# Kernel optimization log

Hardware: AMD Instinct MI355X
Metric: run time of the kernel (lower is better)

Reference implementation:

```python
import jax, jax.numpy as jnp
import numpy as np

B = 8192
N_INPUT = 64
N_OUTPUT = 128
N_HIDDEN = 32
N_TARGETS = 2
N_EXOGS = 3
N_SERIES = N_TARGETS + N_EXOGS  # 5


def _init_linear(k, fan_in, w_shape, b_shape):
    # torch nn.Linear default init: U(-1/sqrt(fan_in), 1/sqrt(fan_in))
    bound = 1.0 / np.sqrt(fan_in)
    kw, kb = jax.random.split(k)
    W = jax.random.uniform(kw, w_shape, jnp.float32, -bound, bound)
    b = jax.random.uniform(kb, b_shape, jnp.float32, -bound, bound)
    return W, b


def setup_inputs() -> dict:
    key = jax.random.key(0)
    ks = jax.random.split(key, 5)
    target = jax.random.normal(ks[0], (B, N_INPUT, N_TARGETS), jnp.float32)
    exog = jax.random.normal(ks[1], (B, N_INPUT + N_OUTPUT, N_EXOGS), jnp.float32)
    # linear1: (n_input*n_series) -> n_targets
    W1, b1 = _init_linear(ks[2], N_INPUT * N_SERIES, (N_TARGETS, N_INPUT * N_SERIES), (N_TARGETS,))
    # linear2: n_series separate (n_input -> n_hidden) linears, stacked
    W2, b2 = _init_linear(ks[3], N_INPUT, (N_SERIES, N_HIDDEN, N_INPUT), (N_SERIES, N_HIDDEN))
    # linear3: (n_hidden*n_series) -> n_targets
    W3, b3 = _init_linear(ks[4], N_HIDDEN * N_SERIES, (N_TARGETS, N_HIDDEN * N_SERIES), (N_TARGETS,))
    return dict(target=target, exog=exog, W1=W1, b1=b1, W2=W2, b2=b2, W3=W3, b3=b3)


def _single_predict(window, ex, W1, b1, W2, b2, W3, b3):
    # window: (B, n_input, n_targets), ex: (B, n_input, n_exogs)
    te = jnp.concatenate([window, ex], axis=2)  # (B, n_input, n_series)
    flat = te.reshape(te.shape[0], -1)          # time-major, series fastest (torch Flatten order)
    out1 = flat @ W1.T + b1                     # (B, n_targets)
    # per-series tiny linears batched via einsum: h[b,i,:] = W2[i] @ te[b,:,i]
    h = jnp.einsum('bti,iht->bih', te, W2) + b2  # (B, n_series, n_hidden)
    h = jax.nn.sigmoid(h).reshape(h.shape[0], -1)  # series-major concat order matches torch.cat
    out2 = h @ W3.T + b3                        # (B, n_targets)
    return out1 + out2 + window[:, -1, :]


def reference(target, exog, W1, b1, W2, b2, W3, b3):
    def step(window, i):
        ex = jax.lax.dynamic_slice_in_dim(exog, i, N_INPUT, axis=1)  # (B, n_input, n_exogs)
        pred = _single_predict(window, ex, W1, b1, W2, b2, W3, b3)   # (B, n_targets)
        window = jnp.concatenate([window[:, 1:, :], pred[:, None, :]], axis=1)
        return window, pred

    _, preds = jax.lax.scan(step, target, jnp.arange(N_OUTPUT))
    return jnp.transpose(preds, (1, 0, 2))  # (B, n_output, n_targets)
```

## Files before the change

kernel.cpp:

```cpp
#include <hip/hip_runtime.h>
#include <math.h>

#define NB 8192
#define NIN 64
#define NOUT 128
#define NHID 32
#define NEXO 3
#define EXROWS 192
#define NTGT 2

typedef float f32x2 __attribute__((ext_vector_type(2)));
typedef float f32x4 __attribute__((ext_vector_type(4)));
typedef int   i32x4 __attribute__((ext_vector_type(4)));
typedef short bf16x8 __attribute__((ext_vector_type(8)));

__device__ __forceinline__ float sigmoidf(float x) {
    return 1.0f / (1.0f + __expf(-x));
}

__device__ __forceinline__ unsigned short f2bf(float x) {
    unsigned int u = __float_as_uint(x);
    unsigned int r = u + 0x7fffu + ((u >> 16) & 1u);
    return (unsigned short)(r >> 16);
}
__device__ __forceinline__ float bf2f(unsigned short h) {
    return __uint_as_float((unsigned int)h << 16);
}

template<int CTRL>
__device__ __forceinline__ float dpp_add(float x) {
    int p = __builtin_amdgcn_update_dpp(0, __float_as_int(x), CTRL, 0xf, 0xf, true);
    return x + __int_as_float(p);
}

#if __has_builtin(__builtin_amdgcn_permlane16_swap)
__device__ __forceinline__ f32x2 xchg16(f32x2 v, int s) {
    auto rx = __builtin_amdgcn_permlane16_swap(__float_as_uint(v.x), __float_as_uint(v.x), false, false);
    auto ry = __builtin_amdgcn_permlane16_swap(__float_as_uint(v.y), __float_as_uint(v.y), false, false);
    f32x2 r;
    r.x = s ? __uint_as_float(rx[0]) : __uint_as_float(rx[1]);
    r.y = s ? __uint_as_float(ry[0]) : __uint_as_float(ry[1]);
    return r;
}
#else
__device__ __forceinline__ f32x2 xchg16(f32x2 v, int s) {
    (void)s;
    f32x2 r;
    r.x = __int_as_float(__builtin_amdgcn_ds_swizzle(__float_as_int(v.x), 0x401f));
    r.y = __int_as_float(__builtin_amdgcn_ds_swizzle(__float_as_int(v.y), 0x401f));
    return r;
}
#endif

__device__ __forceinline__ f32x2 fold32(f32x2 v, int s32) {
    auto rx = __builtin_amdgcn_permlane32_swap(__float_as_uint(v.x), __float_as_uint(v.x), false, false);
    auto ry = __builtin_amdgcn_permlane32_swap(__float_as_uint(v.y), __float_as_uint(v.y), false, false);
    f32x2 o;
    o.x = v.x + (s32 ? __uint_as_float(rx[0]) : __uint_as_float(rx[1]));
    o.y = v.y + (s32 ? __uint_as_float(ry[0]) : __uint_as_float(ry[1]));
    return o;
}

__global__ __launch_bounds__(256, 4) void narx_exog_kernel(
    const float* __restrict__ exog,
    const float* __restrict__ W1, const float* __restrict__ b1,
    const float* __restrict__ W2, const float* __restrict__ b2,
    const float* __restrict__ W3, const float* __restrict__ b3,
    float* __restrict__ E)
{
    __shared__ __align__(16) float exs[NEXO][EXROWS];
    __shared__ __align__(16) unsigned short exrep[NEXO * 8][200];
    __shared__ __align__(16) unsigned short w2bf[NEXO * 32][72];
    __shared__ __align__(16) float2 w1e2[NEXO][NIN];
    __shared__ __align__(16) float b2l[96];
    __shared__ __align__(16) float w3l[2][96];

    const int tid = threadIdx.x;
    const int b = blockIdx.x;
    const float* exb = exog + (size_t)b * (EXROWS * NEXO);

    for (int idx = tid; idx < EXROWS * NEXO; idx += 256) {
        int t = idx / 3;
        int e = idx - t * 3;
        exs[e][t] = exb[idx];
    }
    for (int idx = tid; idx < 6144; idx += 256) {
        int e = idx >> 11;
        int rem = idx & 2047;
        int u = rem >> 6, t = rem & 63;
        w2bf[e * 32 + u][t] = f2bf(W2[(size_t)(64 + e * 32 + u) * NIN + t]);
    }
    for (int idx = tid; idx < 192; idx += 256) {
        int e = idx >> 6, t = idx & 63;
        w1e2[e][t] = make_float2(W1[t * 5 + 2 + e], W1[320 + t * 5 + 2 + e]);
    }
    if (tid < 96)  b2l[tid] = b2[64 + tid];
    for (int idx = tid; idx < 192; idx += 256) {
        int o = idx / 96, u = idx - o * 96;
        w3l[o][u] = W3[o * 160 + 64 + u];
    }
    __syncthreads();

    for (int idx = tid; idx < NEXO * 8 * 192; idx += 256) {
        int e = idx / 1536;
        int rem = idx - e * 1536;
        int r = rem / 192;
        int q = rem - r * 192;
        float v = (q + r < 192) ? exs[e][q + r] : 0.f;
        exrep[e * 8 + r][q] = f2bf(v);
    }
    __syncthreads();

    const int wv = tid >> 6;
    const int l  = tid & 63;
    const int iw = wv * 32;
    const int lg = l >> 4;
    const int col = l & 15;

    float acc0[2] = {0.f, 0.f};
    float acc1[2] = {0.f, 0.f};

    #pragma unroll 1
    for (int e = 0; e < NEXO; ++e) {
        f32x4 b2v[2], w30v[2], w31v[2];
        #pragma unroll
        for (int mt = 0; mt < 2; ++mt) {
            b2v[mt]  = *(const f32x4*)&b2l[e * 32 + mt * 16 + lg * 4];
            w30v[mt] = *(const f32x4*)&w3l[0][e * 32 + mt * 16 + lg * 4];
            w31v[mt] = *(const f32x4*)&w3l[1][e * 32 + mt * 16 + lg * 4];
        }

        f32x4 cacc[2][2];
        #pragma unroll
        for (int mt = 0; mt < 2; ++mt)
            #pragma unroll
            for (int nt = 0; nt < 2; ++nt)
                cacc[mt][nt] = b2v[mt];

        #pragma unroll
        for (int kt = 0; kt < 2; ++kt) {
            bf16x8 af[2], bfr[2];
            #pragma unroll
            for (int mt = 0; mt < 2; ++mt)
                af[mt] = *(const bf16x8*)&w2bf[e * 32 + mt * 16 + col][kt * 32 + lg * 8];
            #pragma unroll
            for (int nt = 0; nt < 2; ++nt)
                bfr[nt] = *(const bf16x8*)&exrep[e * 8 + (l & 7)]
                              [iw + nt * 16 + kt * 32 + lg * 8 + ((l >> 3) & 1) * 8];
            #pragma unroll
            for (int mt = 0; mt < 2; ++mt)
                #pragma unroll
                for (int nt = 0; nt < 2; ++nt)
                    cacc[mt][nt] = __builtin_amdgcn_mfma_f32_16x16x32_bf16(
                        af[mt], bfr[nt], cacc[mt][nt], 0, 0, 0);
        }

        #pragma unroll
        for (int mt = 0; mt < 2; ++mt)
            #pragma unroll
            for (int nt = 0; nt < 2; ++nt) {
                #pragma unroll
                for (int r = 0; r < 4; ++r) {
                    float sg = sigmoidf(cacc[mt][nt][r]);
                    acc0[nt] += w30v[mt][r] * sg;
                    acc1[nt] += w31v[mt][r] * sg;
                }
            }

        const float* exs_e = &exs[e][0];
        #pragma unroll
        for (int dt = 0; dt < 16; ++dt) {
            float2 wv2 = w1e2[e][lg * 16 + dt];
            float x0 = exs_e[iw + l + dt];
            float x1 = exs_e[iw + 16 + l + dt];
            acc0[0] += wv2.x * x0;
            acc1[0] += wv2.y * x0;
            acc0[1] += wv2.x * x1;
            acc1[1] += wv2.y * x1;
        }
    }

    #pragma unroll
    for (int nt = 0; nt < 2; ++nt) {
        acc0[nt] += __shfl_xor(acc0[nt], 16, 64);
        acc0[nt] += __shfl_xor(acc0[nt], 32, 64);
        acc1[nt] += __shfl_xor(acc1[nt], 16, 64);
        acc1[nt] += __shfl_xor(acc1[nt], 32, 64);
    }
    if (lg == 0) {
        const float bias0 = b1[0] + b3[0];
        const float bias1 = b1[1] + b3[1];
        #pragma unroll
        for (int nt = 0; nt < 2; ++nt) {
            int i = iw + nt * 16 + col;
            *(float2*)&E[(size_t)b * (NOUT * NTGT) + i * 2] =
                make_float2(acc0[nt] + bias0, acc1[nt] + bias1);
        }
    }
}

#define CH 8
#define NCH 16

__global__ __launch_bounds__(64) void narx_recur_kernel(
    const float* __restrict__ target,
    const float* __restrict__ W1,
    const float* __restrict__ W2, const float* __restrict__ b2,
    const float* __restrict__ W3,
    float* __restrict__ out)
{
    __shared__ __align__(16) f32x2 yw[NTGT][EXROWS];
    __shared__ __align__(16) unsigned int ypk[NTGT][2][200];
    __shared__ __align__(16) f32x2 ew[NTGT][NOUT];
    __shared__ __align__(16) float pt[64][20];

    const int l = threadIdx.x;
    const int s   = (l >> 4) & 1;
    const int h   = (l & 15) | ((l >> 5) << 4);
    const int u   = s * NHID + h;
    const int s32 = (l >> 5) & 1;
    const size_t bA = (size_t)blockIdx.x * 2;
    const size_t bB = bA + 1;

    for (int i = l; i < NTGT * 2 * 200; i += 64) ((unsigned int*)ypk)[i] = 0u;

    {
        float4 eA = *(const float4*)&out[bA * (NOUT * NTGT) + l * 4];
        float4 eB = *(const float4*)&out[bB * (NOUT * NTGT) + l * 4];
        ew[0][2 * l]     = f32x2{eA.x, eB.x};
        ew[1][2 * l]     = f32x2{eA.y, eB.y};
        ew[0][2 * l + 1] = f32x2{eA.z, eB.z};
        ew[1][2 * l + 1] = f32x2{eA.w, eB.w};
    }
    {
        float2 tA = *(const float2*)&target[bA * (NIN * NTGT) + l * 2];
        float2 tB = *(const float2*)&target[bB * (NIN * NTGT) + l * 2];
        yw[0][l] = f32x2{tA.x, tB.x};
        yw[1][l] = f32x2{tA.y, tB.y};
        float v[2][2] = {{tA.x, tB.x}, {tA.y, tB.y}};
        #pragma unroll
        for (int ss = 0; ss < 2; ++ss)
            #pragma unroll
            for (int q = 0; q < 2; ++q) {
                unsigned short hi = f2bf(v[ss][q]);
                unsigned short lo = f2bf(v[ss][q] - bf2f(hi));
                ypk[ss][q][l] = (unsigned int)hi | ((unsigned int)lo << 16);
            }
    }

    bf16x8 ahf[4][2], alf[4][2];
    {
        const int m0 = l & 15, k0 = (l >> 4) * 8;
        #pragma unroll
        for (int mt = 0; mt < 4; ++mt)
            #pragma unroll
            for (int kt = 0; kt < 2; ++kt) {
                const float* wp = W2 + (size_t)(mt * 16 + m0) * NIN + kt * 32 + k0;
                #pragma unroll
                for (int j = 0; j < 8; ++j) {
                    float x = wp[j];
                    unsigned short hi = f2bf(x);
                    ahf[mt][kt][j] = (short)hi;
                    alf[mt][kt][j] = (short)f2bf(x - bf2f(hi));
                }
            }
    }

    const float bb    = b2[u];
    const float w3own = W3[s * 160 + u];
    const float w3oth = W3[(1 - s) * 160 + u];
    const float wo1a  = W1[s * 320 + (2 * h) * 5 + s];
    const float wo1b  = W1[s * 320 + (2 * h + 1) * 5 + s];
    const float wo2a  = W1[(1 - s) * 320 + (2 * h) * 5 + s];
    const float wo2b  = W1[(1 - s) * 320 + (2 * h + 1) * 5 + s];
    float w2t[7];
    #pragma unroll
    for (int j = 0; j < 7; ++j) w2t[j] = W2[(size_t)u * NIN + 57 + j];

    f32x2* Y = &yw[s][0];
    const f32x2* EV = &ew[s][0];

    const int lag = l & 7;
    const int qb  = (l >> 3) & 1;
    const int bk0 = (l >> 4) * 8;
    const unsigned int* pk0 = &ypk[0][qb][0];
    const unsigned int* pk1 = &ypk[1][qb][0];

    #pragma unroll 1
    for (int c = 0; c < NCH; ++c) {
        const int i0 = c * CH;

        f32x4 acc[4];
        #pragma unroll
        for (int mt = 0; mt < 4; ++mt) acc[mt] = f32x4{0.f, 0.f, 0.f, 0.f};

        #pragma unroll
        for (int kt = 0; kt < 2; ++kt) {
            const int base = i0 + lag + bk0 + kt * 32;
            unsigned int r0[8], r1[8];
            #pragma unroll
            for (int j = 0; j < 8; ++j) { r0[j] = pk0[base + j]; r1[j] = pk1[base + j]; }
            i32x4 h0, l0, h1, l1;
            #pragma unroll
            for (int j2 = 0; j2 < 4; ++j2) {
                h0[j2] = (int)__builtin_amdgcn_perm(r0[2*j2+1], r0[2*j2], 0x05040100u);
                l0[j2] = (int)__builtin_amdgcn_perm(r0[2*j2+1], r0[2*j2], 0x07060302u);
                h1[j2] = (int)__builtin_amdgcn_perm(r1[2*j2+1], r1[2*j2], 0x05040100u);
                l1[j2] = (int)__builtin_amdgcn_perm(r1[2*j2+1], r1[2*j2], 0x07060302u);
            }
            const bf16x8 bh0 = __builtin_bit_cast(bf16x8, h0);
            const bf16x8 bl0 = __builtin_bit_cast(bf16x8, l0);
            const bf16x8 bh1 = __builtin_bit_cast(bf16x8, h1);
            const bf16x8 bl1 = __builtin_bit_cast(bf16x8, l1);
            #pragma unroll
            for (int mt = 0; mt < 4; ++mt) {
                const bf16x8 bh = (mt < 2) ? bh0 : bh1;
                const bf16x8 bl = (mt < 2) ? bl0 : bl1;
                acc[mt] = __builtin_amdgcn_mfma_f32_16x16x32_bf16(ahf[mt][kt], bh, acc[mt], 0, 0, 0);
                acc[mt] = __builtin_amdgcn_mfma_f32_16x16x32_bf16(ahf[mt][kt], bl, acc[mt], 0, 0, 0);
                acc[mt] = __builtin_amdgcn_mfma_f32_16x16x32_bf16(alf[mt][kt], bh, acc[mt], 0, 0, 0);
            }
        }

        {
            const int n = l & 15, r0w = (l >> 4) * 4;
            #pragma unroll
            for (int mt = 0; mt < 4; ++mt)
                #pragma unroll
                for (int r = 0; r < 4; ++r)
                    pt[mt * 16 + r0w + r][n] = acc[mt][r];
        }
        f32x4 pa = *(const f32x4*)&pt[u][0];
        f32x4 pb = *(const f32x4*)&pt[u][4];
        f32x4 pc = *(const f32x4*)&pt[u][8];
        f32x4 pd = *(const f32x4*)&pt[u][12];
        f32x2 P2[CH];
        #pragma unroll
        for (int ci = 0; ci < 4; ++ci) {
            P2[ci]     = f32x2{pa[ci], pc[ci]} + bb;
            P2[ci + 4] = f32x2{pb[ci], pd[ci]} + bb;
        }

        f32x2 ev8[CH];
        #pragma unroll
        for (int q = 0; q < 4; ++q) {
            f32x4 e4 = *(const f32x4*)&EV[i0 + 2 * q];
            ev8[2 * q]     = f32x2{e4[0], e4[1]};
            ev8[2 * q + 1] = f32x2{e4[2], e4[3]};
        }
        f32x2 predprev = Y[i0 + 63];

        #pragma unroll
        for (int ci = 0; ci < CH; ++ci) {
            const int i = i0 + ci;
            const f32x2 y1a = Y[i + 2 * h];
            const f32x2 y1b = Y[i + 2 * h + 1];

            f32x2 sg;
            sg.x = sigmoidf(P2[ci].x);
            sg.y = sigmoidf(P2[ci].y);

            f32x2 va = w3own * sg + wo1a * y1a + wo1b * y1b;
            f32x2 vb = w3oth * sg + wo2a * y1a + wo2b * y1b;

            f32x2 cc = va + xchg16(vb, s);
            cc.x = dpp_add<0xB1>(cc.x);  cc.y = dpp_add<0xB1>(cc.y);
            cc.x = dpp_add<0x4E>(cc.x);  cc.y = dpp_add<0x4E>(cc.y);
            cc.x = dpp_add<0x141>(cc.x); cc.y = dpp_add<0x141>(cc.y);
            cc.x = dpp_add<0x128>(cc.x); cc.y = dpp_add<0x128>(cc.y);
            cc = fold32(cc, s32);

            const f32x2 pred = cc + ev8[ci] + predprev;

            #pragma unroll
            for (int cj = ci + 1; cj < CH; ++cj)
                P2[cj] += w2t[7 - (cj - ci)] * pred;

            if ((l & 47) == 0) Y[i + NIN] = pred;
            if ((l & 47) == 1) {
                unsigned short hA = f2bf(pred.x);
                unsigned short hB = f2bf(pred.y);
                unsigned short lA = f2bf(pred.x - bf2f(hA));
                unsigned short lB = f2bf(pred.y - bf2f(hB));
                ypk[s][0][i + NIN] = (unsigned int)hA | ((unsigned int)lA << 16);
                ypk[s][1][i + NIN] = (unsigned int)hB | ((unsigned int)lB << 16);
            }
            predprev = pred;
        }
    }

    {
        f32x2 a0 = yw[0][NIN + 2 * l];
        f32x2 a1 = yw[1][NIN + 2 * l];
        f32x2 c0 = yw[0][NIN + 2 * l + 1];
        f32x2 c1 = yw[1][NIN + 2 * l + 1];
        *(float4*)&out[bA * (NOUT * NTGT) + l * 4] = make_float4(a0.x, a1.x, c0.x, c1.x);
        *(float4*)&out[bB * (NOUT * NTGT) + l * 4] = make_float4(a0.y, a1.y, c0.y, c1.y);
    }
}

extern "C" void kernel_launch(void* const* d_in, const int* in_sizes, int n_in,
                              void* d_out, int out_size, void* d_ws, size_t ws_size,
                              hipStream_t stream) {
    (void)in_sizes; (void)n_in; (void)out_size; (void)d_ws; (void)ws_size;
    const float* target = (const float*)d_in[0];
    const float* exog   = (const float*)d_in[1];
    const float* W1     = (const float*)d_in[2];
    const float* b1     = (const float*)d_in[3];
    const float* W2     = (const float*)d_in[4];
    const float* b2     = (const float*)d_in[5];
    const float* W3     = (const float*)d_in[6];
    const float* b3     = (const float*)d_in[7];
    float* out = (float*)d_out;

    hipLaunchKernelGGL(narx_exog_kernel, dim3(NB), dim3(256), 0, stream,
                       exog, W1, b1, W2, b2, W3, b3, out);
    hipLaunchKernelGGL(narx_recur_kernel, dim3(NB / 2), dim3(64), 0, stream,
                       target, W1, W2, b2, W3, out);
}
```

Measured before the change: 222.6 us.

## Prepack weights into bf16 MFMA layout in workspace via a one-block kernel

Adds a single-block prepack kernel that converts W2 to bf16 (and hi/lo split) in MFMA fragment order, plus W1/W3/b2 slices, into the workspace each call. The exog kernel then reads W2 fragments directly from global memory instead of staging a converted copy in LDS, which cuts LDS use and per-block conversion work. The recurrence kernel loads pre-split weight fragments. It also moves the bf16 hi/lo packing of predictions out of the serial per-step loop into a batched per-chunk pass. The cost is an extra serial launch and per-fragment global loads in the exog kernel.

```diff
diff --git a/kernel.cpp b/kernel.cpp
--- a/kernel.cpp
+++ b/kernel.cpp
@@ -13,6 +13,11 @@
 typedef float f32x4 __attribute__((ext_vector_type(4)));
 typedef int   i32x4 __attribute__((ext_vector_type(4)));
 typedef short bf16x8 __attribute__((ext_vector_type(8)));
+
+#define WS_W2A  0
+#define WS_W2BH 12288
+#define WS_W2BL 20480
+#define WS_WP   28672
 
 __device__ __forceinline__ float sigmoidf(float x) {
     return 1.0f / (1.0f + __expf(-x));
@@ -61,19 +66,67 @@
     return o;
 }
 
+__global__ __launch_bounds__(256) void narx_prepack_kernel(
+    const float* __restrict__ W1, const float* __restrict__ W2,
+    const float* __restrict__ W3, const float* __restrict__ b2,
+    unsigned char* __restrict__ ws)
+{
+    const int tid = threadIdx.x;
+    unsigned short* w2a  = (unsigned short*)(ws + WS_W2A);
+    unsigned short* w2bh = (unsigned short*)(ws + WS_W2BH);
+    unsigned short* w2bl = (unsigned short*)(ws + WS_W2BL);
+    float* wp = (float*)(ws + WS_WP);
+
+    for (int idx = tid; idx < 6144; idx += 256) {
+        int rem = idx;
+        int j = rem & 7;  rem >>= 3;
+        int lg = rem & 3; rem >>= 2;
+        int col = rem & 15; rem >>= 4;
+        int kt = rem & 1; rem >>= 1;
+        int mt = rem & 1; rem >>= 1;
+        int e = rem;
+        int row = 64 + e * 32 + mt * 16 + col;
+        int t = kt * 32 + lg * 8 + j;
+        w2a[idx] = f2bf(W2[(size_t)row * NIN + t]);
+    }
+    for (int idx = tid; idx < 4096; idx += 256) {
+        int rem = idx;
+        int j = rem & 7;   rem >>= 3;
+        int k0g = rem & 3; rem >>= 2;
+        int m0 = rem & 15; rem >>= 4;
+        int kt = rem & 1;  rem >>= 1;
+        int mt = rem;
+        int row = mt * 16 + m0;
+        int t = kt * 32 + k0g * 8 + j;
+        float x = W2[(size_t)row * NIN + t];
+        unsigned short hi = f2bf(x);
+        w2bh[idx] = hi;
+        w2bl[idx] = f2bf(x - bf2f(hi));
+    }
+    for (int idx = tid; idx < 384; idx += 256) {
+        int e = idx >> 7;
+        int r = idx & 127;
+        int t = r >> 1, o = r & 1;
+        wp[idx] = W1[o * 320 + t * 5 + 2 + e];
+    }
+    if (tid < 192) wp[384 + tid] = W3[(tid / 96) * 160 + 64 + (tid % 96)];
+    if (tid < 96)  wp[576 + tid] = b2[64 + tid];
+}
+
 __global__ __launch_bounds__(256, 4) void narx_exog_kernel(
     const float* __restrict__ exog,
-    const float* __restrict__ W1, const float* __restrict__ b1,
-    const float* __restrict__ W2, const float* __restrict__ b2,
-    const float* __restrict__ W3, const float* __restrict__ b3,
+    const float* __restrict__ b1, const float* __restrict__ b3,
+    const unsigned char* __restrict__ ws,
     float* __restrict__ E)
 {
     __shared__ __align__(16) float exs[NEXO][EXROWS];
     __shared__ __align__(16) unsigned short exrep[NEXO * 8][200];
-    __shared__ __align__(16) unsigned short w2bf[NEXO * 32][72];
     __shared__ __align__(16) float2 w1e2[NEXO][NIN];
+    __shared__ __align__(16) float w3l[2][96];
     __shared__ __align__(16) float b2l[96];
-    __shared__ __align__(16) float w3l[2][96];
+
+    const unsigned short* w2a = (const unsigned short*)(ws + WS_W2A);
+    const float* wp = (const float*)(ws + WS_WP);
 
     const int tid = threadIdx.x;
     const int b = blockIdx.x;
@@ -84,21 +137,9 @@
         int e = idx - t * 3;
         exs[e][t] = exb[idx];
     }
-    for (int idx = tid; idx < 6144; idx += 256) {
-        int e = idx >> 11;
-        int rem = idx & 2047;
-        int u = rem >> 6, t = rem & 63;
-        w2bf[e * 32 + u][t] = f2bf(W2[(size_t)(64 + e * 32 + u) * NIN + t]);
-    }
-    for (int idx = tid; idx < 192; idx += 256) {
-        int e = idx >> 6, t = idx & 63;
-        w1e2[e][t] = make_float2(W1[t * 5 + 2 + e], W1[320 + t * 5 + 2 + e]);
-    }
-    if (tid < 96)  b2l[tid] = b2[64 + tid];
-    for (int idx = tid; idx < 192; idx += 256) {
-        int o = idx / 96, u = idx - o * 96;
-        w3l[o][u] = W3[o * 160 + 64 + u];
-    }
+    for (int idx = tid; idx < 384; idx += 256) ((float*)w1e2)[idx] = wp[idx];
+    if (tid < 192) ((float*)w3l)[tid] = wp[384 + tid];
+    if (tid < 96)  b2l[tid] = wp[576 + tid];
     __syncthreads();
 
     for (int idx = tid; idx < NEXO * 8 * 192; idx += 256) {
@@ -142,7 +183,8 @@
             bf16x8 af[2], bfr[2];
             #pragma unroll
             for (int mt = 0; mt < 2; ++mt)
-                af[mt] = *(const bf16x8*)&w2bf[e * 32 + mt * 16 + col][kt * 32 + lg * 8];
+                af[mt] = *(const bf16x8*)(w2a + ((size_t)((e * 2 + mt) * 2 + kt)) * 512
+                                              + col * 32 + lg * 8);
             #pragma unroll
             for (int nt = 0; nt < 2; ++nt)
                 bfr[nt] = *(const bf16x8*)&exrep[e * 8 + (l & 7)]
@@ -207,12 +249,16 @@
     const float* __restrict__ W1,
     const float* __restrict__ W2, const float* __restrict__ b2,
     const float* __restrict__ W3,
+    const unsigned char* __restrict__ ws,
     float* __restrict__ out)
 {
     __shared__ __align__(16) f32x2 yw[NTGT][EXROWS];
     __shared__ __align__(16) unsigned int ypk[NTGT][2][200];
     __shared__ __align__(16) f32x2 ew[NTGT][NOUT];
     __shared__ __align__(16) float pt[64][20];
+
+    const unsigned short* w2bh = (const unsigned short*)(ws + WS_W2BH);
+    const unsigned short* w2bl = (const unsigned short*)(ws + WS_W2BL);
 
     const int l = threadIdx.x;
     const int s   = (l >> 4) & 1;
@@ -250,19 +296,14 @@
 
     bf16x8 ahf[4][2], alf[4][2];
     {
-        const int m0 = l & 15, k0 = (l >> 4) * 8;
+        const int m0 = l & 15, k0g = l >> 4;
         #pragma unroll
         for (int mt = 0; mt < 4; ++mt)
             #pragma unroll
             for (int kt = 0; kt < 2; ++kt) {
-                const float* wp = W2 + (size_t)(mt * 16 + m0) * NIN + kt * 32 + k0;
-                #pragma unroll
-                for (int j = 0; j < 8; ++j) {
-                    float x = wp[j];
-                    unsigned short hi = f2bf(x);
-                    ahf[mt][kt][j] = (short)hi;
-                    alf[mt][kt][j] = (short)f2bf(x - bf2f(hi));
-                }
+                const int off = ((mt * 2 + kt) * 16 + m0) * 32 + k0g * 8;
+                ahf[mt][kt] = *(const bf16x8*)(w2bh + off);
+                alf[mt][kt] = *(const bf16x8*)(w2bl + off);
             }
     }
 
@@ -290,6 +331,16 @@
     for (int c = 0; c < NCH; ++c) {
         const int i0 = c * CH;
 
+        if (c > 0 && l < 16) {
+            const int ss = l >> 3, j = l & 7;
+            const int row = i0 + 56 + j;
+            f32x2 v = yw[ss][row];
+            unsigned short hA = f2bf(v.x);
+            unsigned short hB = f2bf(v.y);
+            ypk[ss][0][row] = (unsigned int)hA | ((unsigned int)f2bf(v.x - bf2f(hA)) << 16);
+            ypk[ss][1][row] = (unsigned int)hB | ((unsigned int)f2bf(v.y - bf2f(hB)) << 16);
+        }
+
         f32x4 acc[4];
         #pragma unroll
         for (int mt = 0; mt < 4; ++mt) acc[mt] = f32x4{0.f, 0.f, 0.f, 0.f};
@@ -377,14 +428,6 @@
                 P2[cj] += w2t[7 - (cj - ci)] * pred;
 
             if ((l & 47) == 0) Y[i + NIN] = pred;
-            if ((l & 47) == 1) {
-                unsigned short hA = f2bf(pred.x);
-                unsigned short hB = f2bf(pred.y);
-                unsigned short lA = f2bf(pred.x - bf2f(hA));
-                unsigned short lB = f2bf(pred.y - bf2f(hB));
-                ypk[s][0][i + NIN] = (unsigned int)hA | ((unsigned int)lA << 16);
-                ypk[s][1][i + NIN] = (unsigned int)hB | ((unsigned int)lB << 16);
-            }
             predprev = pred;
         }
     }
@@ -402,7 +445,7 @@
 extern "C" void kernel_launch(void* const* d_in, const int* in_sizes, int n_in,
                               void* d_out, int out_size, void* d_ws, size_t ws_size,
                               hipStream_t stream) {
-    (void)in_sizes; (void)n_in; (void)out_size; (void)d_ws; (void)ws_size;
+    (void)in_sizes; (void)n_in; (void)out_size; (void)ws_size;
     const float* target = (const float*)d_in[0];
     const float* exog   = (const float*)d_in[1];
     const float* W1     = (const float*)d_in[2];
@@ -412,9 +455,12 @@
     const float* W3     = (const float*)d_in[6];
     const float* b3     = (const float*)d_in[7];
     float* out = (float*)d_out;
-
+    unsigned char* ws = (unsigned char*)d_ws;
+
+    hipLaunchKernelGGL(narx_prepack_kernel, dim3(1), dim3(256), 0, stream,
+                       W1, W2, W3, b2, ws);
     hipLaunchKernelGGL(narx_exog_kernel, dim3(NB), dim3(256), 0, stream,
-                       exog, W1, b1, W2, b2, W3, b3, out);
+                       exog, b1, b3, ws, out);
     hipLaunchKernelGGL(narx_recur_kernel, dim3(NB / 2), dim3(64), 0, stream,
-                       target, W1, W2, b2, W3, out);
-}
+                       target, W1, W2, b2, W3, ws, out);
+}
```

Result: faster. 211.2 us (-5.1%).
